# Kernel optimization log

Hardware: AMD Instinct MI355X
Metric: run time of the kernel (lower is better)

Reference implementation:

```python
import jax, jax.numpy as jnp
import numpy as np

H = 64   # hidden_dim
E = 5    # num_edge_features
F = 6    # num_node_features
B, W, N = 8, 12, 200
LN_EPS = 1e-5


def _lstm_layer(x, Wih, Whh, bih, bhh):
    # x: [BN, W, Fin] -> full output sequence [BN, W, H] (PyTorch gate order i,f,g,o)
    BN = x.shape[0]
    h0 = jnp.zeros((BN, Whh.shape[1]), x.dtype)
    def step(carry, xt):
        h, c = carry
        g = xt @ Wih.T + h @ Whh.T + (bih + bhh)
        i, f, gg, o = jnp.split(g, 4, axis=-1)
        c = jax.nn.sigmoid(f) * c + jax.nn.sigmoid(i) * jnp.tanh(gg)
        h = jax.nn.sigmoid(o) * jnp.tanh(c)
        return (h, c), h
    _, ys = jax.lax.scan(step, (h0, h0), jnp.swapaxes(x, 0, 1))
    return jnp.swapaxes(ys, 0, 1)


def _layernorm(x, g, b):
    mu = jnp.mean(x, axis=-1, keepdims=True)
    var = jnp.mean(jnp.square(x - mu), axis=-1, keepdims=True)
    return (x - mu) * jax.lax.rsqrt(var + LN_EPS) * g + b


def setup_inputs() -> dict:
    key = jax.random.key(0)
    ks = jax.random.split(key, 32)
    s = 0.05
    d = {
        'node_features': jax.random.normal(ks[0], (B, W, N, F), jnp.float32),
        'edge_features': jax.random.normal(ks[1], (B, W, N, N, E), jnp.float32),
        'adjacency': jax.random.uniform(ks[2], (B, N, N), jnp.float32),
        # LSTM layer 0 (input F) and layer 1 (input H)
        'Wih0': jax.random.normal(ks[3], (4 * H, F), jnp.float32) * s,
        'Whh0': jax.random.normal(ks[4], (4 * H, H), jnp.float32) * s,
        'bih0': jax.random.normal(ks[5], (4 * H,), jnp.float32) * s,
        'bhh0': jax.random.normal(ks[6], (4 * H,), jnp.float32) * s,
        'Wih1': jax.random.normal(ks[7], (4 * H, H), jnp.float32) * s,
        'Whh1': jax.random.normal(ks[8], (4 * H, H), jnp.float32) * s,
        'bih1': jax.random.normal(ks[9], (4 * H,), jnp.float32) * s,
        'bhh1': jax.random.normal(ks[10], (4 * H,), jnp.float32) * s,
        # 2 GCN layers: linear, edge projection, layernorm
        'gcn_W': jax.random.normal(ks[11], (2, H, H), jnp.float32) * s,
        'gcn_b': jax.random.normal(ks[12], (2, H), jnp.float32) * s,
        'ep_W': jax.random.normal(ks[13], (2, H, E), jnp.float32) * s,
        'ep_b': jax.random.normal(ks[14], (2, H), jnp.float32) * s,
        'ln_g': jnp.ones((2, H), jnp.float32),
        'ln_b': jnp.zeros((2, H), jnp.float32),
        # edge MLP: (2H+E) -> H -> H//2 -> 1
        'mlp_W1': jax.random.normal(ks[15], (H, 2 * H + E), jnp.float32) * s,
        'mlp_b1': jax.random.normal(ks[16], (H,), jnp.float32) * s,
        'mlp_W2': jax.random.normal(ks[17], (H // 2, H), jnp.float32) * s,
        'mlp_b2': jax.random.normal(ks[18], (H // 2,), jnp.float32) * s,
        'mlp_W3': jax.random.normal(ks[19], (1, H // 2), jnp.float32) * s,
        'mlp_b3': jax.random.normal(ks[20], (1,), jnp.float32) * s,
    }
    return d


def reference(node_features, edge_features, adjacency,
              Wih0, Whh0, bih0, bhh0, Wih1, Whh1, bih1, bhh1,
              gcn_W, gcn_b, ep_W, ep_b, ln_g, ln_b,
              mlp_W1, mlp_b1, mlp_W2, mlp_b2, mlp_W3, mlp_b3):
    Bn, Wn, Nn, _ = node_features.shape
    # [B,W,N,F] -> [B*N, W, F]
    x = jnp.transpose(node_features, (0, 2, 1, 3)).reshape(Bn * Nn, Wn, -1)
    y0 = _lstm_layer(x, Wih0, Whh0, bih0, bhh0)      # dropout between layers: eval mode (identity)
    y1 = _lstm_layer(y0, Wih1, Whh1, bih1, bhh1)
    h = y1[:, -1, :].reshape(Bn, Nn, H)

    edge_last = edge_features[:, -1]                 # [B,N,N,E]
    for i in range(2):
        edge_h = edge_last @ ep_W[i].T + ep_b[i]     # [B,N,N,H]
        messages = jnp.einsum('bij,bijn->bin', adjacency, edge_h)
        updated = h @ gcn_W[i].T + gcn_b[i] + messages
        h = jax.nn.relu(_layernorm(updated, ln_g[i], ln_b[i]))
        # dropout: eval mode (identity)

    h_i = jnp.broadcast_to(h[:, :, None, :], (Bn, Nn, Nn, H))
    h_j = jnp.broadcast_to(h[:, None, :, :], (Bn, Nn, Nn, H))
    edge_input = jnp.concatenate([h_i, h_j, edge_last], axis=-1)  # [B,N,N,2H+E]
    z = jax.nn.relu(edge_input @ mlp_W1.T + mlp_b1)
    z = jax.nn.relu(z @ mlp_W2.T + mlp_b2)
    logits = (z @ mlp_W3.T + mlp_b3)[..., 0]
    return jax.nn.sigmoid(logits)
```

## Files before the change

kernel.cpp:

```cpp
#include <hip/hip_runtime.h>
#include <math.h>


#define Hd   64
#define Ed   5
#define Fd   6
#define Bd   8
#define Wd   12
#define Nd   200
#define NSEQ (Bd*Nd)
#define NG   (4*Hd)
#define SEQPB 8
#define LNEPS 1e-5f

__device__ __forceinline__ float sigm(float x) { return 1.0f / (1.0f + __expf(-x)); }
__device__ __forceinline__ float tanh_fast(float x) {
  float ax = fabsf(x);
  float t  = __expf(-2.0f * ax);
  float r  = (1.0f - t) / (1.0f + t);
  return copysignf(r, x);
}

__global__ __launch_bounds__(256) void k_prep(
    const float* __restrict__ gcn_W, const float* __restrict__ ep_W,
    const float* __restrict__ W1,
    float* __restrict__ gcnWT, float* __restrict__ epWT,
    float* __restrict__ W1aT, float* __restrict__ W1bT)
{
  int idx = blockIdx.x * 256 + threadIdx.x;
  if (idx < 8192) {
    int round = idx >> 12, rem = idx & 4095;
    int k = rem >> 6, u = rem & 63;
    gcnWT[idx] = gcn_W[round * 4096 + u * 64 + k];
  } else if (idx < 8832) {
    int r0 = idx - 8192;
    int round = r0 / 320, rem = r0 % 320;
    int e = rem >> 6, u = rem & 63;
    epWT[r0] = ep_W[round * 320 + u * Ed + e];
  } else if (idx < 12928) {
    int r0 = idx - 8832;
    int k = r0 >> 6, n = r0 & 63;
    W1aT[r0] = W1[n * 133 + k];
  } else if (idx < 17024) {
    int r0 = idx - 12928;
    int k = r0 >> 6, n = r0 & 63;
    W1bT[r0] = W1[n * 133 + 64 + k];
  }
}

__global__ __launch_bounds__(512, 2) void k_lstm_fused(
    const float* __restrict__ nf,
    const float* __restrict__ Wih0, const float* __restrict__ Whh0,
    const float* __restrict__ bih0, const float* __restrict__ bhh0,
    const float* __restrict__ Wih1, const float* __restrict__ Whh1,
    const float* __restrict__ bih1, const float* __restrict__ bhh1,
    float* __restrict__ hout)
{
  __shared__ float x_sh[SEQPB][Wd * Fd];
  __shared__ float h0_sh[SEQPB][Hd];
  __shared__ float h1_sh[SEQPB][Hd];
  __shared__ float g0_sh[SEQPB][NG];
  __shared__ float g1_sh[SEQPB][NG];

  const int tid  = threadIdx.x;
  const int seq0 = blockIdx.x * SEQPB;
  const int b    = seq0 / Nd;
  const int n0   = seq0 % Nd;

  for (int idx = tid; idx < SEQPB * Wd * Fd; idx += 512) {
    int s = idx / (Wd * Fd), r = idx - s * (Wd * Fd);
    int t = r / Fd, f = r - t * Fd;
    x_sh[s][r] = nf[((b * Wd + t) * Nd + (n0 + s)) * Fd + f];
  }
  ((float*)h0_sh)[tid >= 512 ? 0 : tid] = 0.f;
  ((float*)h1_sh)[tid >= 512 ? 0 : tid] = 0.f;

  const bool isL0 = (tid < 256);
  const int j  = tid & 255;
  const int jt = j >> 6;
  const int u  = tid & 63;
  const int w  = (tid >> 6) & 3;

  float4 wh[16];
  float4 wi1[16];
  float  wx[Fd];
  float  bias;
  if (isL0) {
    const float4* wr = (const float4*)(Whh0 + j * Hd);
    #pragma unroll
    for (int q = 0; q < 16; ++q) wh[q] = wr[q];
    #pragma unroll
    for (int f = 0; f < Fd; ++f) wx[f] = Wih0[j * Fd + f];
    bias = bih0[j] + bhh0[j];
  } else {
    const float4* wr = (const float4*)(Whh1 + j * Hd);
    #pragma unroll
    for (int q = 0; q < 16; ++q) wh[q] = wr[q];
    const float4* xr = (const float4*)(Wih1 + j * Hd);
    #pragma unroll
    for (int q = 0; q < 16; ++q) wi1[q] = xr[q];
    bias = bih1[j] + bhh1[j];
  }

  float cA = 0.f, cB = 0.f;
  float hA = 0.f, hB = 0.f;
  __syncthreads();

  for (int t = 0; t <= Wd; ++t) {
    if (isL0) {
      if (t < Wd) {
        #pragma unroll 2
        for (int s = 0; s < SEQPB; ++s) {
          const float* xp = &x_sh[s][t * Fd];
          float a0 = bias, a1 = 0.f, a2 = 0.f, a3 = 0.f;
          #pragma unroll
          for (int f = 0; f < Fd; ++f) a1 += xp[f] * wx[f];
          const float4* h4 = (const float4*)h0_sh[s];
          #pragma unroll
          for (int q = 0; q < 16; ++q) {
            float4 hv = h4[q];
            float d = hv.x * wh[q].x + hv.y * wh[q].y + hv.z * wh[q].z + hv.w * wh[q].w;
            if ((q & 3) == 0) a0 += d; else if ((q & 3) == 1) a1 += d;
            else if ((q & 3) == 2) a2 += d; else a3 += d;
          }
          float acc = (a0 + a1) + (a2 + a3);
          g0_sh[s][j] = (jt == 2) ? tanh_fast(acc) : sigm(acc);
        }
      }
    } else {
      if (t >= 1) {
        #pragma unroll 2
        for (int s = 0; s < SEQPB; ++s) {
          const float4* y4 = (const float4*)h0_sh[s];
          float xacc = 0.f;
          #pragma unroll
          for (int q = 0; q < 16; ++q) {
            float4 yv = y4[q];
            xacc = fmaf(yv.x, wi1[q].x, xacc);
            xacc = fmaf(yv.y, wi1[q].y, xacc);
            xacc = fmaf(yv.z, wi1[q].z, xacc);
            xacc = fmaf(yv.w, wi1[q].w, xacc);
          }
          xacc += bias;
          float a0 = xacc, a1 = 0.f, a2 = 0.f, a3 = 0.f;
          const float4* h4 = (const float4*)h1_sh[s];
          #pragma unroll
          for (int q = 0; q < 16; ++q) {
            float4 hv = h4[q];
            float d = hv.x * wh[q].x + hv.y * wh[q].y + hv.z * wh[q].z + hv.w * wh[q].w;
            if ((q & 3) == 0) a0 += d; else if ((q & 3) == 1) a1 += d;
            else if ((q & 3) == 2) a2 += d; else a3 += d;
          }
          float acc = (a0 + a1) + (a2 + a3);
          g1_sh[s][j] = (jt == 2) ? tanh_fast(acc) : sigm(acc);
        }
      }
    }
    __syncthreads();

    if (isL0) {
      if (t < Wd) {
        const float* gb = g0_sh[w];
        float iv = gb[u], fv = gb[64 + u], gv = gb[128 + u], ov = gb[192 + u];
        cA = fv * cA + iv * gv;
        hA = ov * tanh_fast(cA);
        h0_sh[w][u] = hA;
        const float* gb2 = g0_sh[w + 4];
        float iv2 = gb2[u], fv2 = gb2[64 + u], gv2 = gb2[128 + u], ov2 = gb2[192 + u];
        cB = fv2 * cB + iv2 * gv2;
        hB = ov2 * tanh_fast(cB);
        h0_sh[w + 4][u] = hB;
      }
    } else {
      if (t >= 1) {
        const float* gb = g1_sh[w];
        float iv = gb[u], fv = gb[64 + u], gv = gb[128 + u], ov = gb[192 + u];
        cA = fv * cA + iv * gv;
        hA = ov * tanh_fast(cA);
        h1_sh[w][u] = hA;
        const float* gb2 = g1_sh[w + 4];
        float iv2 = gb2[u], fv2 = gb2[64 + u], gv2 = gb2[128 + u], ov2 = gb2[192 + u];
        cB = fv2 * cB + iv2 * gv2;
        hB = ov2 * tanh_fast(cB);
        h1_sh[w + 4][u] = hB;
      }
    }
    __syncthreads();
  }

  if (!isL0) {
    hout[(seq0 + w) * Hd + u]     = hA;
    hout[(seq0 + w + 4) * Hd + u] = hB;
  }
}

__global__ __launch_bounds__(256) void k_node(
    const float* __restrict__ ef,    const float* __restrict__ adj,
    const float* __restrict__ h0,
    const float* __restrict__ gcnWT, const float* __restrict__ gcn_b,
    const float* __restrict__ epWT,  const float* __restrict__ ep_b,
    const float* __restrict__ ln_g,  const float* __restrict__ ln_b,
    const float* __restrict__ W1aT,  const float* __restrict__ W1bT,
    const float* __restrict__ b1,
    float* __restrict__ uu, float* __restrict__ vt)
{
  __shared__ float ef_sh[Nd * Ed];
  __shared__ float adj_sh[Nd];
  __shared__ float red[4][6];
  __shared__ float w6[6];
  __shared__ float hcur[Hd];

  const int row = blockIdx.x;
  const int b = row / Nd, i = row % Nd;
  const int tid = threadIdx.x;

  const float* efrow = ef + (size_t)(((b * Wd + (Wd - 1)) * Nd + i)) * (Nd * Ed);
  for (int idx = tid; idx < Nd * Ed; idx += 256) ef_sh[idx] = efrow[idx];
  const float* adjrow = adj + (b * Nd + i) * Nd;
  if (tid < Nd) adj_sh[tid] = adjrow[tid];
  if (tid < Hd) hcur[tid] = h0[row * Hd + tid];
  __syncthreads();

  float p[6] = {0.f, 0.f, 0.f, 0.f, 0.f, 0.f};
  if (tid < Nd) {
    float a = adj_sh[tid];
    p[5] = a;
    #pragma unroll
    for (int k = 0; k < Ed; ++k) p[k] = a * ef_sh[tid * Ed + k];
  }
  #pragma unroll
  for (int k = 0; k < 6; ++k) {
    float v = p[k];
    for (int off = 32; off > 0; off >>= 1) v += __shfl_down(v, off);
    p[k] = v;
  }
  if ((tid & 63) == 0) {
    #pragma unroll
    for (int k = 0; k < 6; ++k) red[tid >> 6][k] = p[k];
  }
  __syncthreads();
  if (tid < 6)
    w6[tid] = red[0][tid] + red[1][tid] + red[2][tid] + red[3][tid];
  __syncthreads();

  const int u = tid & 63;
  #pragma unroll
  for (int round = 0; round < 2; ++round) {
    float hnew = 0.f;
    if (tid < 64) {
      const float* gwT = gcnWT + round * 4096;
      const float* ewT = epWT  + round * 320;
      float acc = gcn_b[round * Hd + u] + w6[5] * ep_b[round * Hd + u];
      #pragma unroll
      for (int e = 0; e < Ed; ++e) acc += w6[e] * ewT[e * 64 + u];
      #pragma unroll 8
      for (int k = 0; k < Hd; ++k) acc += hcur[k] * gwT[k * 64 + u];

      float mu = acc;
      #pragma unroll
      for (int off = 1; off < 64; off <<= 1) mu += __shfl_xor(mu, off);
      mu *= (1.f / 64.f);
      float d = acc - mu;
      float var = d * d;
      #pragma unroll
      for (int off = 1; off < 64; off <<= 1) var += __shfl_xor(var, off);
      var *= (1.f / 64.f);
      float v = d * rsqrtf(var + LNEPS) * ln_g[round * Hd + u] + ln_b[round * Hd + u];
      hnew = fmaxf(v, 0.f);
    }
    __syncthreads();
    if (tid < 64) hcur[tid] = hnew;
    __syncthreads();
  }

  if (tid < 64) {
    float acc = b1[tid];
    #pragma unroll 8
    for (int k = 0; k < Hd; ++k) acc += hcur[k] * W1aT[k * 64 + tid];
    uu[row * Hd + tid] = acc;
  } else if (tid < 128) {
    const int n = tid - 64;
    float acc = 0.f;
    #pragma unroll 8
    for (int k = 0; k < Hd; ++k) acc += hcur[k] * W1bT[k * 64 + n];
    vt[n * NSEQ + row] = acc;
  }
}

__global__ __launch_bounds__(256) void k_mlp(
    const float* __restrict__ ef,
    const float* __restrict__ u, const float* __restrict__ vt,
    const float* __restrict__ W1,
    const float* __restrict__ W2, const float* __restrict__ b2,
    const float* __restrict__ W3, const float* __restrict__ b3,
    float* __restrict__ out)
{
  const int idx = blockIdx.x * 256 + threadIdx.x;
  const int b   = idx / (Nd * Nd);
  const int rem = idx - b * Nd * Nd;
  const int i   = rem / Nd;
  const int jj  = rem - i * Nd;

  const float* e = ef + (((b * Wd + (Wd - 1)) * Nd + i) * Nd + jj) * Ed;
  float e5[Ed];
  #pragma unroll
  for (int q = 0; q < Ed; ++q) e5[q] = e[q];

  const float* ur = u + (b * Nd + i) * Hd;
  const int vcol = b * Nd + jj;

  float z1[64];
  #pragma unroll
  for (int k = 0; k < 64; ++k) {
    float acc = ur[k] + vt[k * NSEQ + vcol];
    const float* w1c = W1 + k * 133 + 128;
    #pragma unroll
    for (int q = 0; q < Ed; ++q) acc += e5[q] * w1c[q];
    z1[k] = fmaxf(acc, 0.f);
  }

  float logit = b3[0];
  #pragma unroll 4
  for (int o = 0; o < 32; ++o) {
    float a0 = b2[o], a1 = 0.f, a2 = 0.f, a3 = 0.f;
    const float* w2 = W2 + o * 64;
    #pragma unroll
    for (int k = 0; k < 64; k += 4) {
      a0 += w2[k]     * z1[k];
      a1 += w2[k + 1] * z1[k + 1];
      a2 += w2[k + 2] * z1[k + 2];
      a3 += w2[k + 3] * z1[k + 3];
    }
    float z2 = fmaxf((a0 + a1) + (a2 + a3), 0.f);
    logit += W3[o] * z2;
  }
  out[idx] = 1.f / (1.f + __expf(-logit));
}

extern "C" void kernel_launch(void* const* d_in, const int* in_sizes, int n_in,
                              void* d_out, int out_size, void* d_ws, size_t ws_size,
                              hipStream_t stream) {
  (void)in_sizes; (void)n_in; (void)out_size; (void)ws_size;
  const float* nf   = (const float*)d_in[0];
  const float* ef   = (const float*)d_in[1];
  const float* adj  = (const float*)d_in[2];
  const float* Wih0 = (const float*)d_in[3];
  const float* Whh0 = (const float*)d_in[4];
  const float* bih0 = (const float*)d_in[5];
  const float* bhh0 = (const float*)d_in[6];
  const float* Wih1 = (const float*)d_in[7];
  const float* Whh1 = (const float*)d_in[8];
  const float* bih1 = (const float*)d_in[9];
  const float* bhh1 = (const float*)d_in[10];
  const float* gcnW = (const float*)d_in[11];
  const float* gcnB = (const float*)d_in[12];
  const float* epW  = (const float*)d_in[13];
  const float* epB  = (const float*)d_in[14];
  const float* lnG  = (const float*)d_in[15];
  const float* lnB  = (const float*)d_in[16];
  const float* W1   = (const float*)d_in[17];
  const float* b1   = (const float*)d_in[18];
  const float* W2   = (const float*)d_in[19];
  const float* b2   = (const float*)d_in[20];
  const float* W3   = (const float*)d_in[21];
  const float* b3   = (const float*)d_in[22];
  float* out = (float*)d_out;

  float* ws   = (float*)d_ws;
  float* h0   = ws;
  float* uu   = h0   + 102400;
  float* vt   = uu   + 102400;
  float* gWT  = vt   + 102400;
  float* eWT  = gWT  + 8192;
  float* W1aT = eWT  + 640;
  float* W1bT = W1aT + 4096;

  k_prep      <<<67,        256, 0, stream>>>(gcnW, epW, W1, gWT, eWT, W1aT, W1bT);
  k_lstm_fused<<<NSEQ/SEQPB,512, 0, stream>>>(nf, Wih0, Whh0, bih0, bhh0,
                                              Wih1, Whh1, bih1, bhh1, h0);
  k_node      <<<1600,      256, 0, stream>>>(ef, adj, h0, gWT, gcnB, eWT, epB,
                                              lnG, lnB, W1aT, W1bT, b1, uu, vt);
  k_mlp       <<<1250,      256, 0, stream>>>(ef, uu, vt, W1, W2, b2, W3, b3, out);
}
```

Measured before the change: 266.0 us.

## Rebalance LSTM fused kernel by moving layer-1 input projection to layer-0 threads

Moves the layer-1 input projection (Wih1·h0) from the layer-1 thread group to the layer-0 threads. Those threads compute it in the same pass over h0 as their recurrent dot product and stage the result in a double-buffered shared array. The pipeline is skewed by one extra step and the Wih0 weights now sit in shared memory. This balances work between the two 256-thread halves, but layer-0 threads now keep 32 float4 weight registers, which raises register pressure, and the loop runs one extra barrier step.

```diff
diff --git a/kernel.cpp b/kernel.cpp
--- a/kernel.cpp
+++ b/kernel.cpp
@@ -57,10 +57,12 @@
     float* __restrict__ hout)
 {
   __shared__ float x_sh[SEQPB][Wd * Fd];
+  __shared__ float wx_sh[NG * Fd];
   __shared__ float h0_sh[SEQPB][Hd];
   __shared__ float h1_sh[SEQPB][Hd];
   __shared__ float g0_sh[SEQPB][NG];
   __shared__ float g1_sh[SEQPB][NG];
+  __shared__ float x1_sh[2][SEQPB][NG];
 
   const int tid  = threadIdx.x;
   const int seq0 = blockIdx.x * SEQPB;
@@ -72,10 +74,12 @@
     int t = r / Fd, f = r - t * Fd;
     x_sh[s][r] = nf[((b * Wd + t) * Nd + (n0 + s)) * Fd + f];
   }
-  ((float*)h0_sh)[tid >= 512 ? 0 : tid] = 0.f;
-  ((float*)h1_sh)[tid >= 512 ? 0 : tid] = 0.f;
-
-  const bool isL0 = (tid < 256);
+  for (int idx = tid; idx < NG * Fd; idx += 512)
+    wx_sh[idx] = Wih0[idx];
+  ((float*)h0_sh)[tid] = 0.f;
+  ((float*)h1_sh)[tid] = 0.f;
+
+  const bool isA = (tid < 256);
   const int j  = tid & 255;
   const int jt = j >> 6;
   const int u  = tid & 63;
@@ -83,38 +87,37 @@
 
   float4 wh[16];
   float4 wi1[16];
-  float  wx[Fd];
-  float  bias;
-  if (isL0) {
+  float  bias0 = 0.f, bias1 = 0.f;
+  if (isA) {
     const float4* wr = (const float4*)(Whh0 + j * Hd);
     #pragma unroll
     for (int q = 0; q < 16; ++q) wh[q] = wr[q];
-    #pragma unroll
-    for (int f = 0; f < Fd; ++f) wx[f] = Wih0[j * Fd + f];
-    bias = bih0[j] + bhh0[j];
+    const float4* xr = (const float4*)(Wih1 + j * Hd);
+    #pragma unroll
+    for (int q = 0; q < 16; ++q) wi1[q] = xr[q];
+    bias0 = bih0[j] + bhh0[j];
+    bias1 = bih1[j] + bhh1[j];
   } else {
     const float4* wr = (const float4*)(Whh1 + j * Hd);
     #pragma unroll
     for (int q = 0; q < 16; ++q) wh[q] = wr[q];
-    const float4* xr = (const float4*)(Wih1 + j * Hd);
-    #pragma unroll
-    for (int q = 0; q < 16; ++q) wi1[q] = xr[q];
-    bias = bih1[j] + bhh1[j];
   }
 
   float cA = 0.f, cB = 0.f;
   float hA = 0.f, hB = 0.f;
+  const float* wxp = wx_sh + j * Fd;
   __syncthreads();
 
-  for (int t = 0; t <= Wd; ++t) {
-    if (isL0) {
+  for (int t = 0; t <= Wd + 1; ++t) {
+    if (isA) {
       if (t < Wd) {
         #pragma unroll 2
         for (int s = 0; s < SEQPB; ++s) {
           const float* xp = &x_sh[s][t * Fd];
-          float a0 = bias, a1 = 0.f, a2 = 0.f, a3 = 0.f;
+          float a0 = bias0, a1 = 0.f, a2 = 0.f, a3 = 0.f;
           #pragma unroll
-          for (int f = 0; f < Fd; ++f) a1 += xp[f] * wx[f];
+          for (int f = 0; f < Fd; ++f) a1 += xp[f] * wxp[f];
+          float xacc = 0.f;
           const float4* h4 = (const float4*)h0_sh[s];
           #pragma unroll
           for (int q = 0; q < 16; ++q) {
@@ -122,27 +125,37 @@
             float d = hv.x * wh[q].x + hv.y * wh[q].y + hv.z * wh[q].z + hv.w * wh[q].w;
             if ((q & 3) == 0) a0 += d; else if ((q & 3) == 1) a1 += d;
             else if ((q & 3) == 2) a2 += d; else a3 += d;
+            xacc = fmaf(hv.x, wi1[q].x, xacc);
+            xacc = fmaf(hv.y, wi1[q].y, xacc);
+            xacc = fmaf(hv.z, wi1[q].z, xacc);
+            xacc = fmaf(hv.w, wi1[q].w, xacc);
           }
           float acc = (a0 + a1) + (a2 + a3);
           g0_sh[s][j] = (jt == 2) ? tanh_fast(acc) : sigm(acc);
+          if (t >= 1) x1_sh[t & 1][s][j] = xacc + bias1;
+        }
+      } else if (t == Wd) {
+        #pragma unroll 2
+        for (int s = 0; s < SEQPB; ++s) {
+          float xacc = 0.f;
+          const float4* h4 = (const float4*)h0_sh[s];
+          #pragma unroll
+          for (int q = 0; q < 16; ++q) {
+            float4 hv = h4[q];
+            xacc = fmaf(hv.x, wi1[q].x, xacc);
+            xacc = fmaf(hv.y, wi1[q].y, xacc);
+            xacc = fmaf(hv.z, wi1[q].z, xacc);
+            xacc = fmaf(hv.w, wi1[q].w, xacc);
+          }
+          x1_sh[t & 1][s][j] = xacc + bias1;
         }
       }
     } else {
-      if (t >= 1) {
+      if (t >= 2) {
         #pragma unroll 2
         for (int s = 0; s < SEQPB; ++s) {
-          const float4* y4 = (const float4*)h0_sh[s];
-          float xacc = 0.f;
-          #pragma unroll
-          for (int q = 0; q < 16; ++q) {
-            float4 yv = y4[q];
-            xacc = fmaf(yv.x, wi1[q].x, xacc);
-            xacc = fmaf(yv.y, wi1[q].y, xacc);
-            xacc = fmaf(yv.z, wi1[q].z, xacc);
-            xacc = fmaf(yv.w, wi1[q].w, xacc);
-          }
-          xacc += bias;
-          float a0 = xacc, a1 = 0.f, a2 = 0.f, a3 = 0.f;
+          float a0 = x1_sh[(t - 1) & 1][s][j];
+          float a1 = 0.f, a2 = 0.f, a3 = 0.f;
           const float4* h4 = (const float4*)h1_sh[s];
           #pragma unroll
           for (int q = 0; q < 16; ++q) {
@@ -158,7 +171,7 @@
     }
     __syncthreads();
 
-    if (isL0) {
+    if (isA) {
       if (t < Wd) {
         const float* gb = g0_sh[w];
         float iv = gb[u], fv = gb[64 + u], gv = gb[128 + u], ov = gb[192 + u];
@@ -172,7 +185,7 @@
         h0_sh[w + 4][u] = hB;
       }
     } else {
-      if (t >= 1) {
+      if (t >= 2) {
         const float* gb = g1_sh[w];
         float iv = gb[u], fv = gb[64 + u], gv = gb[128 + u], ov = gb[192 + u];
         cA = fv * cA + iv * gv;
@@ -188,7 +201,7 @@
     __syncthreads();
   }
 
-  if (!isL0) {
+  if (!isA) {
     hout[(seq0 + w) * Hd + u]     = hA;
     hout[(seq0 + w + 4) * Hd + u] = hB;
   }
```

Result: slower. 349.1 us (+31.3%).
